# Performance work log

Hardware: AMD Instinct MI355X
Metric: run time of the kernel (lower is better)

The kernel has to match this reference:

```python
import jax, jax.numpy as jnp
import numpy as np

N = 100000   # nodes
E = 1600000  # edges
EPS = 1e-5


def _gcn_conv(x, W, b, src, dst, dinv):
    # PyG GCNConv with self-loops: out_i = sum_{j->i} d_j^-1/2 d_i^-1/2 (x_j W) + d_i^-1 (x_i W) + b
    h = x @ W                                   # [N, out]
    coef = dinv[src] * dinv[dst]                # [E]
    agg = jax.ops.segment_sum(h[src] * coef[:, None], dst, num_segments=N)
    agg = agg + h * (dinv * dinv)[:, None]      # self-loop term
    return agg + b


def _bn_eval(x, gamma, beta, mean, var):
    return (x - mean) * jax.lax.rsqrt(var + EPS) * gamma + beta


def setup_inputs() -> dict:
    key = jax.random.key(0)
    ks = jax.random.split(key, 8)
    F_IN, H, C = 128, 256, 32
    inp = {
        "x": jax.random.normal(ks[0], (N, F_IN), dtype=jnp.float32),
        "edge_index": jax.random.randint(ks[1], (2, E), 0, N, dtype=jnp.int64),
        # layer 1
        "W1": jax.random.normal(ks[2], (F_IN, H), dtype=jnp.float32) / np.sqrt(F_IN),
        "b1": jnp.zeros((H,), jnp.float32),
        "g1": jnp.ones((H,), jnp.float32),
        "be1": jnp.zeros((H,), jnp.float32),
        "m1": jax.random.normal(ks[3], (H,), dtype=jnp.float32) * 0.1,
        "v1": jnp.ones((H,), jnp.float32),
        # layer 2
        "W2": jax.random.normal(ks[4], (H, H), dtype=jnp.float32) / np.sqrt(H),
        "b2": jnp.zeros((H,), jnp.float32),
        "g2": jnp.ones((H,), jnp.float32),
        "be2": jnp.zeros((H,), jnp.float32),
        "m2": jax.random.normal(ks[5], (H,), dtype=jnp.float32) * 0.1,
        "v2": jnp.ones((H,), jnp.float32),
        # layer 3
        "W3": jax.random.normal(ks[6], (H, C), dtype=jnp.float32) / np.sqrt(H),
        "b3": jnp.zeros((C,), jnp.float32),
    }
    return inp


def reference(x, edge_index, W1, b1, g1, be1, m1, v1,
              W2, b2, g2, be2, m2, v2, W3, b3):
    src, dst = edge_index[0], edge_index[1]
    # degree with self-loops: in-degree + 1
    deg = jnp.zeros((N,), x.dtype).at[dst].add(1.0) + 1.0
    dinv = jax.lax.rsqrt(deg)

    h = _gcn_conv(x, W1, b1, src, dst, dinv)
    h = jax.nn.relu(_bn_eval(h, g1, be1, m1, v1))
    h = _gcn_conv(h, W2, b2, src, dst, dinv)
    h = jax.nn.relu(_bn_eval(h, g2, be2, m2, v2))
    h = _gcn_conv(h, W3, b3, src, dst, dinv)
    return jax.nn.sigmoid(h)
```

## Files before the change

### kernel.cpp

```cpp
#include <hip/hip_runtime.h>
#include <math.h>

typedef unsigned short u16;
typedef unsigned char u8;
typedef unsigned int u32;
typedef __attribute__((ext_vector_type(8))) __bf16 bfx8;
typedef __attribute__((ext_vector_type(4))) float f32x4;
typedef __attribute__((ext_vector_type(2))) float f32x2;
typedef __attribute__((ext_vector_type(8))) unsigned short us8;
typedef __attribute__((ext_vector_type(4))) unsigned short us4;

__device__ inline float bf2f(u16 u) {
    union { unsigned int i; float f; } v;
    v.i = ((unsigned int)u) << 16;
    return v.f;
}
__device__ inline u16 f2bf(float f) {
    union { float f; unsigned int i; } v;
    v.f = f;
    unsigned int b = v.i;
    return (u16)((b + 0x7FFFu + ((b >> 16) & 1u)) >> 16);
}


__global__ __launch_bounds__(256) void k_hist(const int* __restrict__ ei,
                                              u32* __restrict__ cnt_pb,
                                              int E, int NB, int NBLK) {
    __shared__ u32 h[256];
    int blk = blockIdx.x, tid = threadIdx.x;
    h[tid] = 0;
    __syncthreads();
    int eend = min(E, (blk + 1) * 2048);
    for (int e = blk * 2048 + tid; e < eend; e += 256) {
        int d = ei[E + e];
        atomicAdd(&h[d >> 9], 1u);
    }
    __syncthreads();
    if (tid < NB) cnt_pb[(size_t)tid * NBLK + blk] = h[tid];
}

__global__ __launch_bounds__(1024) void k_scanb(const u32* __restrict__ cnt_pb,
                                                u32* __restrict__ bases_pb,
                                                u32* __restrict__ bkt_tot,
                                                int NBLK) {
    __shared__ u32 lds[1024];
    int b = blockIdx.x, t = threadIdx.x;
    u32 v = (t < NBLK) ? cnt_pb[(size_t)b * NBLK + t] : 0u;
    lds[t] = v;
    __syncthreads();
    for (int off = 1; off < 1024; off <<= 1) {
        u32 x = lds[t];
        u32 y = (t >= off) ? lds[t - off] : 0u;
        __syncthreads();
        lds[t] = x + y;
        __syncthreads();
    }
    if (t < NBLK) bases_pb[(size_t)b * NBLK + t] = lds[t] - v;
    if (t == NBLK - 1) bkt_tot[b] = lds[t];
}

__global__ __launch_bounds__(256) void k_scant(const u32* __restrict__ bkt_tot,
                                               u32* __restrict__ bkt_base,
                                               int* __restrict__ row_ptr,
                                               int NB, int N, int E) {
    __shared__ u32 lds[256];
    int t = threadIdx.x;
    u32 v = (t < NB) ? bkt_tot[t] : 0u;
    lds[t] = v;
    __syncthreads();
    for (int off = 1; off < 256; off <<= 1) {
        u32 x = lds[t];
        u32 y = (t >= off) ? lds[t - off] : 0u;
        __syncthreads();
        lds[t] = x + y;
        __syncthreads();
    }
    if (t < NB) bkt_base[t] = lds[t] - v;
    if (t == 0) row_ptr[N] = E;
}

__global__ __launch_bounds__(256) void k_scatter2(const int* __restrict__ ei,
                                                  const u32* __restrict__ bases_pb,
                                                  const u32* __restrict__ bkt_base,
                                                  u32* __restrict__ bkt_edges,
                                                  int E, int NB, int NBLK) {
    __shared__ u32 cur[256];
    __shared__ u32 bb[256];
    int blk = blockIdx.x, tid = threadIdx.x;
    if (tid < NB) {
        cur[tid] = bases_pb[(size_t)tid * NBLK + blk];
        bb[tid] = bkt_base[tid];
    }
    __syncthreads();
    int eend = min(E, (blk + 1) * 2048);
    for (int e = blk * 2048 + tid; e < eend; e += 256) {
        int s = ei[e];
        int d = ei[E + e];
        int b = d >> 9;
        int dl = d & 511;
        u32 off = atomicAdd(&cur[b], 1u);
        bkt_edges[bb[b] + off] = (u32)s | ((u32)dl << 17);
    }
}

__global__ __launch_bounds__(512) void k_bucket(const u32* __restrict__ bkt_edges,
                                                const u32* __restrict__ bkt_base,
                                                const u32* __restrict__ bkt_tot,
                                                int* __restrict__ row_ptr,
                                                float* __restrict__ dinv,
                                                int* __restrict__ csr_src,
                                                int N) {
    __shared__ u32 lcnt[512];
    __shared__ u32 lscan[512];
    int b = blockIdx.x, t = threadIdx.x;
    int node0 = b << 9;
    int es = (int)bkt_base[b];
    int ce = (int)bkt_tot[b];
    lcnt[t] = 0;
    __syncthreads();
    for (int i = t; i < ce; i += 512) {
        u32 p = bkt_edges[es + i];
        atomicAdd(&lcnt[p >> 17], 1u);
    }
    __syncthreads();
    lscan[t] = lcnt[t];
    __syncthreads();
    for (int off = 1; off < 512; off <<= 1) {
        u32 x = lscan[t];
        u32 y = (t >= off) ? lscan[t - off] : 0u;
        __syncthreads();
        lscan[t] = x + y;
        __syncthreads();
    }
    u32 excl = lscan[t] - lcnt[t];
    int node = node0 + t;
    if (node < N) {
        row_ptr[node] = es + (int)excl;
        dinv[node] = rsqrtf((float)lcnt[t] + 1.0f);
    }
    __syncthreads();
    lscan[t] = excl;
    __syncthreads();
    for (int i = t; i < ce; i += 512) {
        u32 p = bkt_edges[es + i];
        int dl = (int)(p >> 17);
        int src = (int)(p & 0x1FFFFu);
        u32 pos = atomicAdd(&lscan[dl], 1u);
        csr_src[es + pos] = src;
    }
}


__global__ void k_bnfold(const float* __restrict__ b, const float* __restrict__ g,
                         const float* __restrict__ be, const float* __restrict__ m,
                         const float* __restrict__ v, float* __restrict__ s,
                         float* __restrict__ t, int H) {
    int i = blockIdx.x * blockDim.x + threadIdx.x;
    if (i < H) {
        float sc = g[i] * rsqrtf(v[i] + 1e-5f);
        s[i] = sc;
        t[i] = (b[i] - m[i]) * sc + be[i];
    }
}

__global__ void k_w2bf(const float* __restrict__ W, u16* __restrict__ Wt, int K, int F) {
    int i = blockIdx.x * blockDim.x + threadIdx.x;
    if (i < K * F) {
        int k = i / F, f = i % F;
        Wt[(size_t)f * K + k] = f2bf(W[i]);
    }
}

__global__ void k_x2f8(const float* __restrict__ x, u8* __restrict__ xq,
                       const float* __restrict__ dinv, int n4) {
    int i = blockIdx.x * blockDim.x + threadIdx.x;
    if (i < n4) {
        float d = dinv[i >> 5];
        float4 v = *(const float4*)(x + (size_t)i * 4);
        unsigned int pk = 0;
        pk = __builtin_amdgcn_cvt_pk_fp8_f32(v.x * d, v.y * d, pk, false);
        pk = __builtin_amdgcn_cvt_pk_fp8_f32(v.z * d, v.w * d, pk, true);
        *(unsigned int*)(xq + (size_t)i * 4) = pk;
    }
}

template<int K, int FT, int MODE, int MINW>
__global__ __launch_bounds__(256, MINW) void g_mfma_lds(
    const u16* __restrict__ A, const u16* __restrict__ Wt,
    void* __restrict__ Cv, int M, int Ftot,
    const float* __restrict__ s, const float* __restrict__ t,
    const float* __restrict__ dinv, int nTiles)
{
    constexpr int BK  = 128;
    constexpr int SA  = BK + 8;
    constexpr int NH  = K / BK;
    constexpr int NKH = BK / 32;
    constexpr int NF  = FT / 16;
    constexpr int EB  = (MODE == 3) ? 1 : 2;
    constexpr int SCB = FT * EB + 16;

    __shared__ u16 Asmem[2][64 * SA];
    __shared__ u8  Cs8[64 * SCB];

    int tid = threadIdx.x;
    int w = tid >> 6, l = tid & 63;
    int lr = l & 15, koff8 = (l >> 4) * 8;
    int col0 = blockIdx.y * FT;

    bfx8 bfr[NH][NKH][NF];
    {
        const u16* wp = Wt + (size_t)(col0 + lr) * K + koff8;
        #pragma unroll
        for (int h = 0; h < NH; ++h)
            #pragma unroll
            for (int kk = 0; kk < NKH; ++kk)
                #pragma unroll
                for (int c = 0; c < NF; ++c)
                    bfr[h][kk][c] = *(const bfx8*)(wp + (size_t)c * 16 * K + h * BK + kk * 32);
    }

    int myT = (blockIdx.x < nTiles) ? ((nTiles - 1 - (int)blockIdx.x) / (int)gridDim.x + 1) : 0;
    int NM = myT * NH;
    if (NM == 0) return;

    f32x4 acc[NF];
    #pragma unroll
    for (int c = 0; c < NF; ++c) acc[c] = (f32x4){0.f, 0.f, 0.f, 0.f};

    us8 rga[4];

    {
        int row0 = blockIdx.x * 64;
        #pragma unroll
        for (int j = 0; j < 4; ++j) {
            int cid = j * 256 + tid;
            int row = cid >> 4, ch = cid & 15;
            int gr = row0 + row; if (gr > M - 1) gr = M - 1;
            rga[j] = *(const us8*)(A + (size_t)gr * K + 0 * BK + ch * 8);
        }
        #pragma unroll
        for (int j = 0; j < 4; ++j) {
            int cid = j * 256 + tid;
            int row = cid >> 4, ch = cid & 15;
            *(us8*)&Asmem[0][row * SA + ch * 8] = rga[j];
        }
        if (NM > 1) {
            constexpr int gt1 = 1 / NH, h1 = 1 % NH;
            int r0 = (blockIdx.x + gt1 * gridDim.x) * 64;
            #pragma unroll
            for (int j = 0; j < 4; ++j) {
                int cid = j * 256 + tid;
                int row = cid >> 4, ch = cid & 15;
                int gr = r0 + row; if (gr > M - 1) gr = M - 1;
                rga[j] = *(const us8*)(A + (size_t)gr * K + h1 * BK + ch * 8);
            }
        }
    }
    __syncthreads();

    int cur = 0, gm = 0;
    for (int ti = 0; ti < myT; ++ti) {
        int row0g = (blockIdx.x + ti * gridDim.x) * 64;
        #pragma unroll
        for (int h = 0; h < NH; ++h) {
            const u16* ab = &Asmem[cur][0];
            #pragma unroll
            for (int kk = 0; kk < NKH; ++kk) {
                bfx8 af = *(const bfx8*)(ab + (w * 16 + lr) * SA + koff8 + kk * 32);
                #pragma unroll
                for (int c = 0; c < NF; ++c)
                    acc[c] = __builtin_amdgcn_mfma_f32_16x16x32_bf16(af, bfr[h][kk][c], acc[c], 0, 0, 0);
            }
            if (h == NH - 1) {
                int orow = w * 16 + (l >> 4) * 4;
                float dr[4];
                #pragma unroll
                for (int r = 0; r < 4; ++r) {
                    int grow = row0g + orow + r;
                    dr[r] = (MODE == 2) ? 1.f : ((grow < M) ? dinv[grow] : 0.f);
                }
                #pragma unroll
                for (int c = 0; c < NF; ++c) {
                    int gc = col0 + c * 16 + lr;
                    float sc = (MODE == 2) ? 0.f : s[gc];
                    float tc = (MODE == 2) ? 0.f : t[gc];
                    #pragma unroll
                    for (int r = 0; r < 4; ++r) {
                        float v = acc[c][r];
                        if (MODE != 2) v = fmaxf(v * sc + tc, 0.f) * dr[r];
                        if (MODE == 3) {
                            int enc = __builtin_amdgcn_cvt_pk_fp8_f32(v, v, 0, false);
                            Cs8[(orow + r) * SCB + (c * 16 + lr)] = (u8)(enc & 0xff);
                        } else {
                            *(u16*)&Cs8[(orow + r) * SCB + (c * 16 + lr) * 2] = f2bf(v);
                        }
                    }
                    acc[c] = (f32x4){0.f, 0.f, 0.f, 0.f};
                }
            }
            __syncthreads();
            if (gm + 1 < NM) {
                #pragma unroll
                for (int j = 0; j < 4; ++j) {
                    int cid = j * 256 + tid;
                    int row = cid >> 4, ch = cid & 15;
                    *(us8*)&Asmem[cur ^ 1][row * SA + ch * 8] = rga[j];
                }
            }
            if (h == NH - 1) {
                constexpr int CPR = (FT * EB) / 16;
                constexpr int CPT = (64 * CPR) / 256;
                u8* C8 = (u8*)Cv;
                #pragma unroll
                for (int j = 0; j < CPT; ++j) {
                    int cid = j * 256 + tid;
                    int crow = cid / CPR;
                    int cb = (cid % CPR) * 16;
                    int grow = row0g + crow;
                    if (grow < M) {
                        us8 vv = *(const us8*)&Cs8[crow * SCB + cb];
                        *(us8*)(C8 + (size_t)grow * Ftot * EB + (size_t)col0 * EB + cb) = vv;
                    }
                }
            }
            if (gm + 2 < NM) {
                int g2 = gm + 2;
                int gt2 = g2 / NH, h2 = g2 % NH;
                int r0 = (blockIdx.x + gt2 * gridDim.x) * 64;
                #pragma unroll
                for (int j = 0; j < 4; ++j) {
                    int cid = j * 256 + tid;
                    int row = cid >> 4, ch = cid & 15;
                    int gr = r0 + row; if (gr > M - 1) gr = M - 1;
                    rga[j] = *(const us8*)(A + (size_t)gr * K + h2 * BK + ch * 8);
                }
            }
            __syncthreads();
            cur ^= 1; ++gm;
        }
    }
}

__global__ __launch_bounds__(256) void agg_x(const u8* __restrict__ in,
                                             u16* __restrict__ outp,
                                             const int* __restrict__ row_ptr,
                                             const int* __restrict__ csr_src,
                                             const float* __restrict__ dinv,
                                             int nnodes) {
    int tid = threadIdx.x;
    int wv = tid >> 6, lane = tid & 63;
    int half = lane >> 5, l32 = lane & 31;
    int node = (blockIdx.x * 4 + wv) * 2 + half;
    if (node >= nnodes) return;
    int off = l32 * 4;
    const u8* bp = in + off;
    float a0, a1, a2, a3;
    {
        unsigned int q = *(const unsigned int*)(in + (size_t)node * 128 + off);
        f32x2 p;
        p = __builtin_amdgcn_cvt_pk_f32_fp8(q, false); a0 = p[0]; a1 = p[1];
        p = __builtin_amdgcn_cvt_pk_f32_fp8(q, true);  a2 = p[0]; a3 = p[1];
    }
    int e = row_ptr[node], e1 = row_ptr[node + 1];
    for (; e + 8 <= e1; e += 8) {
        int sx[8];
        #pragma unroll
        for (int q = 0; q < 8; ++q) sx[q] = csr_src[e + q];
        unsigned int vv[8];
        #pragma unroll
        for (int q = 0; q < 8; ++q) vv[q] = *(const unsigned int*)(bp + (size_t)sx[q] * 128);
        #pragma unroll
        for (int q = 0; q < 8; ++q) {
            f32x2 p;
            p = __builtin_amdgcn_cvt_pk_f32_fp8(vv[q], false); a0 += p[0]; a1 += p[1];
            p = __builtin_amdgcn_cvt_pk_f32_fp8(vv[q], true);  a2 += p[0]; a3 += p[1];
        }
    }
    for (; e < e1; ++e) {
        int s0 = csr_src[e];
        unsigned int v0 = *(const unsigned int*)(bp + (size_t)s0 * 128);
        f32x2 p;
        p = __builtin_amdgcn_cvt_pk_f32_fp8(v0, false); a0 += p[0]; a1 += p[1];
        p = __builtin_amdgcn_cvt_pk_f32_fp8(v0, true);  a2 += p[0]; a3 += p[1];
    }
    float d = dinv[node];
    us4 o;
    o.x = f2bf(a0 * d); o.y = f2bf(a1 * d); o.z = f2bf(a2 * d); o.w = f2bf(a3 * d);
    *(us4*)(outp + (size_t)node * 128 + l32 * 4) = o;
}

__global__ __launch_bounds__(256) void agg_h(const u8* __restrict__ in,
                                             u16* __restrict__ outp,
                                             const int* __restrict__ row_ptr,
                                             const int* __restrict__ csr_src,
                                             const float* __restrict__ dinv,
                                             int nnodes) {
    int tid = threadIdx.x;
    int wv = tid >> 6, lane = tid & 63;
    int half = lane >> 5, l32 = lane & 31;
    int node = (blockIdx.x * 4 + wv) * 2 + half;
    if (node >= nnodes) return;
    int off = l32 * 8;
    const u8* bp = in + off;
    float acc[8];
    {
        uint2 q = *(const uint2*)(in + (size_t)node * 256 + off);
        f32x2 p;
        p = __builtin_amdgcn_cvt_pk_f32_fp8(q.x, false); acc[0] = p[0]; acc[1] = p[1];
        p = __builtin_amdgcn_cvt_pk_f32_fp8(q.x, true);  acc[2] = p[0]; acc[3] = p[1];
        p = __builtin_amdgcn_cvt_pk_f32_fp8(q.y, false); acc[4] = p[0]; acc[5] = p[1];
        p = __builtin_amdgcn_cvt_pk_f32_fp8(q.y, true);  acc[6] = p[0]; acc[7] = p[1];
    }
    int e = row_ptr[node], e1 = row_ptr[node + 1];
    for (; e + 8 <= e1; e += 8) {
        int sx[8];
        #pragma unroll
        for (int q = 0; q < 8; ++q) sx[q] = csr_src[e + q];
        uint2 vv[8];
        #pragma unroll
        for (int q = 0; q < 8; ++q) vv[q] = *(const uint2*)(bp + (size_t)sx[q] * 256);
        #pragma unroll
        for (int q = 0; q < 8; ++q) {
            f32x2 p;
            p = __builtin_amdgcn_cvt_pk_f32_fp8(vv[q].x, false); acc[0] += p[0]; acc[1] += p[1];
            p = __builtin_amdgcn_cvt_pk_f32_fp8(vv[q].x, true);  acc[2] += p[0]; acc[3] += p[1];
            p = __builtin_amdgcn_cvt_pk_f32_fp8(vv[q].y, false); acc[4] += p[0]; acc[5] += p[1];
            p = __builtin_amdgcn_cvt_pk_f32_fp8(vv[q].y, true);  acc[6] += p[0]; acc[7] += p[1];
        }
    }
    for (; e < e1; ++e) {
        int s0 = csr_src[e];
        uint2 v0 = *(const uint2*)(bp + (size_t)s0 * 256);
        f32x2 p;
        p = __builtin_amdgcn_cvt_pk_f32_fp8(v0.x, false); acc[0] += p[0]; acc[1] += p[1];
        p = __builtin_amdgcn_cvt_pk_f32_fp8(v0.x, true);  acc[2] += p[0]; acc[3] += p[1];
        p = __builtin_amdgcn_cvt_pk_f32_fp8(v0.y, false); acc[4] += p[0]; acc[5] += p[1];
        p = __builtin_amdgcn_cvt_pk_f32_fp8(v0.y, true);  acc[6] += p[0]; acc[7] += p[1];
    }
    float d = dinv[node];
    us8 o;
    #pragma unroll
    for (int j = 0; j < 8; ++j) o[j] = f2bf(acc[j] * d);
    *(us8*)(outp + (size_t)node * 256 + off) = o;
}

__global__ __launch_bounds__(256) void agg32_sig(const u16* __restrict__ z,
                                                 float* __restrict__ out,
                                                 const int* __restrict__ row_ptr,
                                                 const int* __restrict__ csr_src,
                                                 const float* __restrict__ dinv,
                                                 const float* __restrict__ b3,
                                                 int nnodes) {
    int tid = threadIdx.x;
    int wv = tid >> 6, lane = tid & 63;
    int half = lane >> 5, l32 = lane & 31;
    int node = (blockIdx.x * 4 + wv) * 2 + half;
    if (node >= nnodes) return;
    float acc = bf2f(z[(size_t)node * 32 + l32]);
    int e = row_ptr[node], e1 = row_ptr[node + 1];
    for (; e + 4 <= e1; e += 4) {
        int s0 = csr_src[e], s1 = csr_src[e + 1], s2 = csr_src[e + 2], s3 = csr_src[e + 3];
        float z0 = bf2f(z[(size_t)s0 * 32 + l32]);
        float z1 = bf2f(z[(size_t)s1 * 32 + l32]);
        float z2 = bf2f(z[(size_t)s2 * 32 + l32]);
        float z3v = bf2f(z[(size_t)s3 * 32 + l32]);
        acc += z0 + z1 + z2 + z3v;
    }
    for (; e < e1; ++e) {
        acc += bf2f(z[(size_t)csr_src[e] * 32 + l32]);
    }
    acc = acc * dinv[node] + b3[l32];
    out[(size_t)node * 32 + l32] = 1.f / (1.f + expf(-acc));
}


extern "C" void kernel_launch(void* const* d_in, const int* in_sizes, int n_in,
                              void* d_out, int out_size, void* d_ws, size_t ws_size,
                              hipStream_t stream) {
    const float* x  = (const float*)d_in[0];
    const int*   ei = (const int*)d_in[1];
    const float* W1 = (const float*)d_in[2];
    const float* b1 = (const float*)d_in[3];
    const float* g1 = (const float*)d_in[4];
    const float* be1 = (const float*)d_in[5];
    const float* m1 = (const float*)d_in[6];
    const float* v1 = (const float*)d_in[7];
    const float* W2 = (const float*)d_in[8];
    const float* b2 = (const float*)d_in[9];
    const float* g2 = (const float*)d_in[10];
    const float* be2 = (const float*)d_in[11];
    const float* m2 = (const float*)d_in[12];
    const float* v2 = (const float*)d_in[13];
    const float* W3 = (const float*)d_in[14];
    const float* b3 = (const float*)d_in[15];
    float* out = (float*)d_out;

    const int N = in_sizes[0] / 128;
    const int E = in_sizes[1] / 2;

    const int NB = (N + 511) >> 9;
    const int NBLK = (E + 2047) / 2048;

    char* w = (char*)d_ws;
    auto alloc = [&](size_t bytes) -> void* {
        void* p = (void*)w;
        w += (bytes + 255) & ~(size_t)255;
        return p;
    };
    int* row_ptr   = (int*)alloc((size_t)(N + 1) * 4);
    float* dinv    = (float*)alloc((size_t)N * 4);
    u32* cnt_pb    = (u32*)alloc((size_t)NB * NBLK * 4);
    u32* bases_pb  = (u32*)alloc((size_t)NB * NBLK * 4);
    u32* bkt_tot   = (u32*)alloc((size_t)NB * 4);
    u32* bkt_base  = (u32*)alloc((size_t)NB * 4);
    u32* bkt_edges = (u32*)alloc((size_t)E * 4);
    float* s1 = (float*)alloc(256 * 4);
    float* t1 = (float*)alloc(256 * 4);
    float* s2 = (float*)alloc(256 * 4);
    float* t2 = (float*)alloc(256 * 4);
    u16* Wt1 = (u16*)alloc((size_t)128 * 256 * 2);
    u16* Wt2 = (u16*)alloc((size_t)256 * 256 * 2);
    u16* Wt3 = (u16*)alloc((size_t)256 * 32 * 2);
    int* csr_src = (int*)alloc((size_t)E * 4);
    u8*  xq   = (u8*)alloc((size_t)N * 128);
    u16* bufA = (u16*)alloc((size_t)N * 256 * 2);
    u16* bufB = (u16*)alloc((size_t)N * 256 * 2);
    u8*  h1q  = (u8*)alloc((size_t)N * 256);
    u16* z3 = (u16*)xq;

    int nT = (N + 63) / 64;
    int gagg = (N + 7) / 8;

    k_hist<<<NBLK, 256, 0, stream>>>(ei, cnt_pb, E, NB, NBLK);
    k_scanb<<<NB, 1024, 0, stream>>>(cnt_pb, bases_pb, bkt_tot, NBLK);
    k_scant<<<1, 256, 0, stream>>>(bkt_tot, bkt_base, row_ptr, NB, N, E);
    k_scatter2<<<NBLK, 256, 0, stream>>>(ei, bases_pb, bkt_base, bkt_edges, E, NB, NBLK);
    k_bucket<<<NB, 512, 0, stream>>>(bkt_edges, bkt_base, bkt_tot, row_ptr, dinv, csr_src, N);

    k_bnfold<<<1, 256, 0, stream>>>(b1, g1, be1, m1, v1, s1, t1, 256);
    k_bnfold<<<1, 256, 0, stream>>>(b2, g2, be2, m2, v2, s2, t2, 256);
    k_w2bf<<<(128 * 256 + 255) / 256, 256, 0, stream>>>(W1, Wt1, 128, 256);
    k_w2bf<<<(256 * 256 + 255) / 256, 256, 0, stream>>>(W2, Wt2, 256, 256);
    k_w2bf<<<(256 * 32 + 255) / 256, 256, 0, stream>>>(W3, Wt3, 256, 32);
    k_x2f8<<<(N * 128 / 4 + 255) / 256, 256, 0, stream>>>(x, xq, dinv, N * 128 / 4);

    agg_x<<<gagg, 256, 0, stream>>>(xq, bufA, row_ptr, csr_src, dinv, N);
    g_mfma_lds<128, 64, 3, 2><<<dim3(128, 4), 256, 0, stream>>>(
        bufA, Wt1, (void*)h1q, N, 256, s1, t1, dinv, nT);

    agg_h<<<gagg, 256, 0, stream>>>(h1q, bufA, row_ptr, csr_src, dinv, N);
    g_mfma_lds<256, 64, 1, 2><<<dim3(128, 4), 256, 0, stream>>>(
        bufA, Wt2, (void*)bufB, N, 256, s2, t2, dinv, nT);

    g_mfma_lds<256, 32, 2, 2><<<dim3(512, 1), 256, 0, stream>>>(
        bufB, Wt3, (void*)z3, N, 32, (const float*)nullptr, (const float*)nullptr,
        (const float*)nullptr, nT);
    agg32_sig<<<gagg, 256, 0, stream>>>(z3, out, row_ptr, csr_src, dinv, b3, N);
}
```

Before: 283.5 us.

## Store aggregated activations and layer-2 output in FP8, decode to bf16 in GEMM

The aggregation kernels now write their outputs as packed FP8 instead of bf16. The second GEMM also emits FP8 (mode 3) rather than bf16. The GEMM kernel gains an AFP8 path that loads FP8 tiles and decodes them to bf16 while writing to LDS. This halves the bytes written by the aggregation kernels and read by the GEMMs, at the cost of extra per-element conversion work and further precision loss on the intermediate activations.

```diff
diff --git a/kernel.cpp b/kernel.cpp
--- a/kernel.cpp
+++ b/kernel.cpp
@@ -20,6 +20,18 @@
     v.f = f;
     unsigned int b = v.i;
     return (u16)((b + 0x7FFFu + ((b >> 16) & 1u)) >> 16);
+}
+__device__ inline u32 bits_of(float f) {
+    union { float f; u32 i; } v; v.f = f; return v.i;
+}
+__device__ inline u32 pkbf(float a, float b) {
+    return (bits_of(a) >> 16) | (bits_of(b) & 0xffff0000u);
+}
+__device__ inline void dec4(u32 d, u32& lo, u32& hi) {
+    f32x2 a = __builtin_amdgcn_cvt_pk_f32_fp8(d, false);
+    f32x2 b = __builtin_amdgcn_cvt_pk_f32_fp8(d, true);
+    lo = pkbf(a[0], a[1]);
+    hi = pkbf(b[0], b[1]);
 }
 
 
@@ -184,9 +196,9 @@
     }
 }
 
-template<int K, int FT, int MODE, int MINW>
+template<int K, int FT, int MODE, bool AFP8, int MINW>
 __global__ __launch_bounds__(256, MINW) void g_mfma_lds(
-    const u16* __restrict__ A, const u16* __restrict__ Wt,
+    const void* __restrict__ Av, const u16* __restrict__ Wt,
     void* __restrict__ Cv, int M, int Ftot,
     const float* __restrict__ s, const float* __restrict__ t,
     const float* __restrict__ dinv, int nTiles)
@@ -198,10 +210,14 @@
     constexpr int NF  = FT / 16;
     constexpr int EB  = (MODE == 3) ? 1 : 2;
     constexpr int SCB = FT * EB + 16;
+    constexpr int EBa = AFP8 ? 1 : 2;
+    constexpr int CR  = (BK * EBa) / 16;
+    constexpr int LIT = (64 * CR) / 256;
 
     __shared__ u16 Asmem[2][64 * SA];
     __shared__ u8  Cs8[64 * SCB];
 
+    const u8* Ab = (const u8*)Av;
     int tid = threadIdx.x;
     int w = tid >> 6, l = tid & 63;
     int lr = l & 15, koff8 = (l >> 4) * 8;
@@ -227,34 +243,43 @@
     #pragma unroll
     for (int c = 0; c < NF; ++c) acc[c] = (f32x4){0.f, 0.f, 0.f, 0.f};
 
-    us8 rga[4];
-
-    {
-        int row0 = blockIdx.x * 64;
-        #pragma unroll
-        for (int j = 0; j < 4; ++j) {
+    uint4 rga[LIT];
+
+    auto loadA = [&](int r0, int hh) {
+        #pragma unroll
+        for (int j = 0; j < LIT; ++j) {
             int cid = j * 256 + tid;
-            int row = cid >> 4, ch = cid & 15;
-            int gr = row0 + row; if (gr > M - 1) gr = M - 1;
-            rga[j] = *(const us8*)(A + (size_t)gr * K + 0 * BK + ch * 8);
+            int row = cid / CR, ch = cid % CR;
+            int gr = r0 + row; if (gr > M - 1) gr = M - 1;
+            rga[j] = *(const uint4*)(Ab + (size_t)gr * K * EBa + (size_t)hh * BK * EBa + ch * 16);
         }
-        #pragma unroll
-        for (int j = 0; j < 4; ++j) {
+    };
+    auto writeA = [&](int buf) {
+        #pragma unroll
+        for (int j = 0; j < LIT; ++j) {
             int cid = j * 256 + tid;
-            int row = cid >> 4, ch = cid & 15;
-            *(us8*)&Asmem[0][row * SA + ch * 8] = rga[j];
-        }
-        if (NM > 1) {
-            constexpr int gt1 = 1 / NH, h1 = 1 % NH;
-            int r0 = (blockIdx.x + gt1 * gridDim.x) * 64;
-            #pragma unroll
-            for (int j = 0; j < 4; ++j) {
-                int cid = j * 256 + tid;
-                int row = cid >> 4, ch = cid & 15;
-                int gr = r0 + row; if (gr > M - 1) gr = M - 1;
-                rga[j] = *(const us8*)(A + (size_t)gr * K + h1 * BK + ch * 8);
+            int row = cid / CR, ch = cid % CR;
+            if (!AFP8) {
+                *(uint4*)&Asmem[buf][row * SA + ch * 8] = rga[j];
+            } else {
+                u32 w0, w1, w2, w3, w4, w5, w6, w7;
+                dec4(rga[j].x, w0, w1);
+                dec4(rga[j].y, w2, w3);
+                dec4(rga[j].z, w4, w5);
+                dec4(rga[j].w, w6, w7);
+                uint4 lo4; lo4.x = w0; lo4.y = w1; lo4.z = w2; lo4.w = w3;
+                uint4 hi4; hi4.x = w4; hi4.y = w5; hi4.z = w6; hi4.w = w7;
+                *(uint4*)&Asmem[buf][row * SA + ch * 16] = lo4;
+                *(uint4*)&Asmem[buf][row * SA + ch * 16 + 8] = hi4;
             }
         }
+    };
+
+    loadA(blockIdx.x * 64, 0);
+    writeA(0);
+    if (NM > 1) {
+        constexpr int gt1 = 1 / NH, h1 = 1 % NH;
+        loadA((blockIdx.x + gt1 * gridDim.x) * 64, h1);
     }
     __syncthreads();
 
@@ -299,14 +324,7 @@
                 }
             }
             __syncthreads();
-            if (gm + 1 < NM) {
-                #pragma unroll
-                for (int j = 0; j < 4; ++j) {
-                    int cid = j * 256 + tid;
-                    int row = cid >> 4, ch = cid & 15;
-                    *(us8*)&Asmem[cur ^ 1][row * SA + ch * 8] = rga[j];
-                }
-            }
+            if (gm + 1 < NM) writeA(cur ^ 1);
             if (h == NH - 1) {
                 constexpr int CPR = (FT * EB) / 16;
                 constexpr int CPT = (64 * CPR) / 256;
@@ -326,14 +344,7 @@
             if (gm + 2 < NM) {
                 int g2 = gm + 2;
                 int gt2 = g2 / NH, h2 = g2 % NH;
-                int r0 = (blockIdx.x + gt2 * gridDim.x) * 64;
-                #pragma unroll
-                for (int j = 0; j < 4; ++j) {
-                    int cid = j * 256 + tid;
-                    int row = cid >> 4, ch = cid & 15;
-                    int gr = r0 + row; if (gr > M - 1) gr = M - 1;
-                    rga[j] = *(const us8*)(A + (size_t)gr * K + h2 * BK + ch * 8);
-                }
+                loadA((blockIdx.x + gt2 * gridDim.x) * 64, h2);
             }
             __syncthreads();
             cur ^= 1; ++gm;
@@ -342,7 +353,7 @@
 }
 
 __global__ __launch_bounds__(256) void agg_x(const u8* __restrict__ in,
-                                             u16* __restrict__ outp,
+                                             u8* __restrict__ outp,
                                              const int* __restrict__ row_ptr,
                                              const int* __restrict__ csr_src,
                                              const float* __restrict__ dinv,
@@ -384,13 +395,14 @@
         p = __builtin_amdgcn_cvt_pk_f32_fp8(v0, true);  a2 += p[0]; a3 += p[1];
     }
     float d = dinv[node];
-    us4 o;
-    o.x = f2bf(a0 * d); o.y = f2bf(a1 * d); o.z = f2bf(a2 * d); o.w = f2bf(a3 * d);
-    *(us4*)(outp + (size_t)node * 128 + l32 * 4) = o;
+    u32 pk = 0;
+    pk = __builtin_amdgcn_cvt_pk_fp8_f32(a0 * d, a1 * d, pk, false);
+    pk = __builtin_amdgcn_cvt_pk_fp8_f32(a2 * d, a3 * d, pk, true);
+    *(u32*)(outp + (size_t)node * 128 + off) = pk;
 }
 
 __global__ __launch_bounds__(256) void agg_h(const u8* __restrict__ in,
-                                             u16* __restrict__ outp,
+                                             u8* __restrict__ outp,
                                              const int* __restrict__ row_ptr,
                                              const int* __restrict__ csr_src,
                                              const float* __restrict__ dinv,
@@ -438,10 +450,13 @@
         p = __builtin_amdgcn_cvt_pk_f32_fp8(v0.y, true);  acc[6] += p[0]; acc[7] += p[1];
     }
     float d = dinv[node];
-    us8 o;
-    #pragma unroll
-    for (int j = 0; j < 8; ++j) o[j] = f2bf(acc[j] * d);
-    *(us8*)(outp + (size_t)node * 256 + off) = o;
+    u32 w0 = 0, w1 = 0;
+    w0 = __builtin_amdgcn_cvt_pk_fp8_f32(acc[0] * d, acc[1] * d, w0, false);
+    w0 = __builtin_amdgcn_cvt_pk_fp8_f32(acc[2] * d, acc[3] * d, w0, true);
+    w1 = __builtin_amdgcn_cvt_pk_fp8_f32(acc[4] * d, acc[5] * d, w1, false);
+    w1 = __builtin_amdgcn_cvt_pk_fp8_f32(acc[6] * d, acc[7] * d, w1, true);
+    uint2 o; o.x = w0; o.y = w1;
+    *(uint2*)(outp + (size_t)node * 256 + off) = o;
 }
 
 __global__ __launch_bounds__(256) void agg32_sig(const u16* __restrict__ z,
@@ -523,9 +538,10 @@
     u16* Wt3 = (u16*)alloc((size_t)256 * 32 * 2);
     int* csr_src = (int*)alloc((size_t)E * 4);
     u8*  xq   = (u8*)alloc((size_t)N * 128);
-    u16* bufA = (u16*)alloc((size_t)N * 256 * 2);
-    u16* bufB = (u16*)alloc((size_t)N * 256 * 2);
+    u8*  xa   = (u8*)alloc((size_t)N * 128);
     u8*  h1q  = (u8*)alloc((size_t)N * 256);
+    u8*  h1a  = (u8*)alloc((size_t)N * 256);
+    u8*  h2q  = (u8*)alloc((size_t)N * 256);
     u16* z3 = (u16*)xq;
 
     int nT = (N + 63) / 64;
@@ -544,16 +560,16 @@
     k_w2bf<<<(256 * 32 + 255) / 256, 256, 0, stream>>>(W3, Wt3, 256, 32);
     k_x2f8<<<(N * 128 / 4 + 255) / 256, 256, 0, stream>>>(x, xq, dinv, N * 128 / 4);
 
-    agg_x<<<gagg, 256, 0, stream>>>(xq, bufA, row_ptr, csr_src, dinv, N);
-    g_mfma_lds<128, 64, 3, 2><<<dim3(128, 4), 256, 0, stream>>>(
-        bufA, Wt1, (void*)h1q, N, 256, s1, t1, dinv, nT);
-
-    agg_h<<<gagg, 256, 0, stream>>>(h1q, bufA, row_ptr, csr_src, dinv, N);
-    g_mfma_lds<256, 64, 1, 2><<<dim3(128, 4), 256, 0, stream>>>(
-        bufA, Wt2, (void*)bufB, N, 256, s2, t2, dinv, nT);
-
-    g_mfma_lds<256, 32, 2, 2><<<dim3(512, 1), 256, 0, stream>>>(
-        bufB, Wt3, (void*)z3, N, 32, (const float*)nullptr, (const float*)nullptr,
-        (const float*)nullptr, nT);
+    agg_x<<<gagg, 256, 0, stream>>>(xq, xa, row_ptr, csr_src, dinv, N);
+    g_mfma_lds<128, 64, 3, true, 2><<<dim3(128, 4), 256, 0, stream>>>(
+        (const void*)xa, Wt1, (void*)h1q, N, 256, s1, t1, dinv, nT);
+
+    agg_h<<<gagg, 256, 0, stream>>>(h1q, h1a, row_ptr, csr_src, dinv, N);
+    g_mfma_lds<256, 64, 3, true, 2><<<dim3(128, 4), 256, 0, stream>>>(
+        (const void*)h1a, Wt2, (void*)h2q, N, 256, s2, t2, dinv, nT);
+
+    g_mfma_lds<256, 32, 2, true, 2><<<dim3(512, 1), 256, 0, stream>>>(
+        (const void*)h2q, Wt3, (void*)z3, N, 32, (const float*)nullptr,
+        (const float*)nullptr, (const float*)nullptr, nT);
     agg32_sig<<<gagg, 256, 0, stream>>>(z3, out, row_ptr, csr_src, dinv, b3, N);
 }
```

After: 282.5 us. About the same (-0.4%).
